# Optimization experiments

Hardware: AMD Instinct MI355X
Metric: run time of the kernel (lower is better)

## Reference

```python
import jax, jax.numpy as jnp
import numpy as np

FEATURE_LIST = [222, 27, 373, 283, 26, 7]
EMB_HID = 6
TN, UN, TF = 2000, 50000, 16


def setup_inputs() -> dict:
    key = jax.random.key(0)
    ks = jax.random.split(key, 4 + len(FEATURE_LIST))
    T_static = jax.random.normal(ks[0], (TN, TF), dtype=jnp.float32)
    # per-column categorical indices, each in-range for its table
    cols = [jax.random.randint(jax.random.fold_in(ks[1], i), (UN,), 0, sz)
            for i, sz in enumerate(FEATURE_LIST)]
    U_static = jnp.stack(cols, axis=1).astype(jnp.int64)  # [UN, 6]
    team_user_matrix = jax.random.randint(ks[2], (TN, UN), 0, 2, dtype=jnp.int32)
    inp = {"T_static": T_static, "U_static": U_static,
           "team_user_matrix": team_user_matrix}
    # embedding tables, xavier_uniform with gain=sqrt(2)
    for i, sz in enumerate(FEATURE_LIST):
        bound = np.sqrt(2.0) * np.sqrt(6.0 / (sz + EMB_HID))
        inp[f"emb{i}"] = jax.random.uniform(ks[3 + i], (sz, EMB_HID),
                                            minval=-bound, maxval=bound,
                                            dtype=jnp.float32)
    return inp


def reference(T_static, U_static, team_user_matrix,
              emb0, emb1, emb2, emb3, emb4, emb5):
    tables = [emb0, emb1, emb2, emb3, emb4, emb5]
    # gather per-feature embeddings and concat -> [UN, 6*emb_hid]
    U_emb = jnp.concatenate(
        [t[U_static[:, i]] for i, t in enumerate(tables)], axis=-1)
    mask = (team_user_matrix == 1).astype(U_emb.dtype)        # [TN, UN]
    counts = jnp.sum(mask, axis=1, keepdims=True)             # [TN, 1]
    # masked mean over each team's users == (mask @ U_emb) / counts
    T_emb = jnp.matmul(mask, U_emb) / counts                  # [TN, 36]
    return jnp.concatenate([T_static, T_emb], axis=-1)        # [TN, TF+36]
```

## Files before the change

kernel.cpp:

```cpp
#include <hip/hip_runtime.h>
#include <hip/hip_bf16.h>

#define TN 2000
#define UN 50000
#define TF 16
#define NCOL 48
#define UNP 50016
#define KSTEPS 1563
#define KCHUNKS 48
#define SPC 33
#define MTILES 125

typedef __attribute__((ext_vector_type(8))) short short8;
typedef __attribute__((ext_vector_type(4))) float f32x4;

__device__ inline unsigned short f2bf(float f) {
    unsigned int x = __float_as_uint(f);
    x += 0x7FFFu + ((x >> 16) & 1u);
    return (unsigned short)(x >> 16);
}

__global__ void build_uembT(const int* __restrict__ U,
                            const float* __restrict__ e0, const float* __restrict__ e1,
                            const float* __restrict__ e2, const float* __restrict__ e3,
                            const float* __restrict__ e4, const float* __restrict__ e5,
                            unsigned short* __restrict__ UT) {
    int u = blockIdx.x * 256 + threadIdx.x;
    if (u >= UNP) return;
    const float* tabs[6] = {e0, e1, e2, e3, e4, e5};
    if (u < UN) {
        #pragma unroll
        for (int f = 0; f < 6; ++f) {
            int idx = U[u * 6 + f];
            #pragma unroll
            for (int h = 0; h < 6; ++h)
                UT[(size_t)(f * 6 + h) * UNP + u] = f2bf(tabs[f][idx * 6 + h]);
        }
        UT[(size_t)36 * UNP + u] = 0x3F80;
    } else {
        #pragma unroll
        for (int c = 0; c < 37; ++c) UT[(size_t)c * UNP + u] = 0;
    }
    #pragma unroll
    for (int c = 37; c < NCOL; ++c) UT[(size_t)c * UNP + u] = 0;
}

__global__ __launch_bounds__(256) void masked_gemm(
        const int* __restrict__ mask, const unsigned short* __restrict__ UT,
        float* __restrict__ accum) {
    int wave = threadIdx.x >> 6;
    int lane = threadIdx.x & 63;
    int mtile = blockIdx.x * 4 + wave;
    if (mtile >= MTILES) return;
    int m0 = mtile * 16;
    int r  = lane & 15;
    int g8 = (lane >> 4) * 8;

    int ks0 = blockIdx.y * SPC;
    int ks1 = ks0 + SPC; if (ks1 > KSTEPS) ks1 = KSTEPS;

    f32x4 acc0 = {0.f, 0.f, 0.f, 0.f};
    f32x4 acc1 = {0.f, 0.f, 0.f, 0.f};
    f32x4 acc2 = {0.f, 0.f, 0.f, 0.f};

    const int* arow = mask + (size_t)(m0 + r) * UN;
    const unsigned short* b0 = UT + (size_t)(r)      * UNP;
    const unsigned short* b1 = UT + (size_t)(r + 16) * UNP;
    const unsigned short* b2 = UT + (size_t)(r + 32) * UNP;

    for (int ks = ks0; ks < ks1; ++ks) {
        int gk = ks * 32 + g8;
        short8 a;
        if (gk < UN) {
            const int4* p = (const int4*)(arow + gk);
            int4 v0 = p[0], v1 = p[1];
            int v[8] = {v0.x, v0.y, v0.z, v0.w, v1.x, v1.y, v1.z, v1.w};
            #pragma unroll
            for (int j = 0; j < 8; ++j) a[j] = (v[j] == 1) ? (short)0x3F80 : (short)0;
        } else {
            #pragma unroll
            for (int j = 0; j < 8; ++j) a[j] = (short)0;
        }
        short8 f0 = *(const short8*)(b0 + gk);
        short8 f1 = *(const short8*)(b1 + gk);
        short8 f2 = *(const short8*)(b2 + gk);
        acc0 = __builtin_amdgcn_mfma_f32_16x16x32_bf16(a, f0, acc0, 0, 0, 0);
        acc1 = __builtin_amdgcn_mfma_f32_16x16x32_bf16(a, f1, acc1, 0, 0, 0);
        acc2 = __builtin_amdgcn_mfma_f32_16x16x32_bf16(a, f2, acc2, 0, 0, 0);
    }

    int row0 = m0 + (lane >> 4) * 4;
    int col  = lane & 15;
    #pragma unroll
    for (int reg = 0; reg < 4; ++reg)
        atomicAdd(&accum[(size_t)(row0 + reg) * NCOL + col], acc0[reg]);
    #pragma unroll
    for (int reg = 0; reg < 4; ++reg)
        atomicAdd(&accum[(size_t)(row0 + reg) * NCOL + col + 16], acc1[reg]);
    if (col < 5) {
        #pragma unroll
        for (int reg = 0; reg < 4; ++reg)
            atomicAdd(&accum[(size_t)(row0 + reg) * NCOL + col + 32], acc2[reg]);
    }
}

__global__ void finalize(const float* __restrict__ T_static,
                         const float* __restrict__ accum,
                         float* __restrict__ out) {
    int t = blockIdx.x;
    int c = threadIdx.x;
    if (c >= TF + 36) return;
    float v;
    if (c < TF) {
        v = T_static[(size_t)t * TF + c];
    } else {
        float cnt = accum[(size_t)t * NCOL + 36];
        v = accum[(size_t)t * NCOL + (c - TF)] / cnt;
    }
    out[(size_t)t * (TF + 36) + c] = v;
}

extern "C" void kernel_launch(void* const* d_in, const int* in_sizes, int n_in,
                              void* d_out, int out_size, void* d_ws, size_t ws_size,
                              hipStream_t stream) {
    const float* T_static = (const float*)d_in[0];
    const int*   U_static = (const int*)d_in[1];
    const int*   mask     = (const int*)d_in[2];
    const float* e0 = (const float*)d_in[3];
    const float* e1 = (const float*)d_in[4];
    const float* e2 = (const float*)d_in[5];
    const float* e3 = (const float*)d_in[6];
    const float* e4 = (const float*)d_in[7];
    const float* e5 = (const float*)d_in[8];
    float* out = (float*)d_out;

    unsigned short* UT = (unsigned short*)d_ws;
    size_t ut_bytes = (size_t)NCOL * UNP * sizeof(unsigned short);
    float* accum = (float*)((char*)d_ws + ut_bytes);

    hipMemsetAsync(accum, 0, (size_t)TN * NCOL * sizeof(float), stream);
    build_uembT<<<dim3((UNP + 255) / 256), dim3(256), 0, stream>>>(
        U_static, e0, e1, e2, e3, e4, e5, UT);
    masked_gemm<<<dim3(32, KCHUNKS), dim3(256), 0, stream>>>(mask, UT, accum);
    finalize<<<dim3(TN), dim3(64), 0, stream>>>(T_static, accum, out);
}
```

Measured before the change: 590.2 us.

## Replace atomics with per-chunk partials, parallelize embedding build, peel tail step

```diff
diff --git a/kernel.cpp b/kernel.cpp
--- a/kernel.cpp
+++ b/kernel.cpp
@@ -7,6 +7,7 @@
 #define NCOL 48
 #define UNP 50016
 #define KSTEPS 1563
+#define KFULL 1562
 #define KCHUNKS 48
 #define SPC 33
 #define MTILES 125
@@ -26,28 +27,37 @@
                             const float* __restrict__ e4, const float* __restrict__ e5,
                             unsigned short* __restrict__ UT) {
     int u = blockIdx.x * 256 + threadIdx.x;
+    int c = blockIdx.y;
     if (u >= UNP) return;
-    const float* tabs[6] = {e0, e1, e2, e3, e4, e5};
+    unsigned short val = 0;
     if (u < UN) {
-        #pragma unroll
-        for (int f = 0; f < 6; ++f) {
+        if (c < 36) {
+            int f = c / 6, h = c - f * 6;
+            const float* t = (f == 0) ? e0 : (f == 1) ? e1 : (f == 2) ? e2
+                           : (f == 3) ? e3 : (f == 4) ? e4 : e5;
             int idx = U[u * 6 + f];
-            #pragma unroll
-            for (int h = 0; h < 6; ++h)
-                UT[(size_t)(f * 6 + h) * UNP + u] = f2bf(tabs[f][idx * 6 + h]);
+            val = f2bf(t[idx * 6 + h]);
+        } else if (c == 36) {
+            val = 0x3F80;
         }
-        UT[(size_t)36 * UNP + u] = 0x3F80;
-    } else {
-        #pragma unroll
-        for (int c = 0; c < 37; ++c) UT[(size_t)c * UNP + u] = 0;
     }
+    UT[(size_t)c * UNP + u] = val;
+}
+
+__device__ inline short8 mask_to_bf16(const int v[8]) {
+    union { short8 s; int i[4]; } a;
     #pragma unroll
-    for (int c = 37; c < NCOL; ++c) UT[(size_t)c * UNP + u] = 0;
+    for (int j = 0; j < 4; ++j) {
+        int lo = (v[2 * j]     == 1) ? 0x3F80     : 0;
+        int hi = (v[2 * j + 1] == 1) ? 0x3F800000 : 0;
+        a.i[j] = lo | hi;
+    }
+    return a.s;
 }
 
 __global__ __launch_bounds__(256) void masked_gemm(
         const int* __restrict__ mask, const unsigned short* __restrict__ UT,
-        float* __restrict__ accum) {
+        float* __restrict__ partial) {
     int wave = threadIdx.x >> 6;
     int lane = threadIdx.x & 63;
     int mtile = blockIdx.x * 4 + wave;
@@ -55,31 +65,43 @@
     int m0 = mtile * 16;
     int r  = lane & 15;
     int g8 = (lane >> 4) * 8;
+    int ky = blockIdx.y;
 
-    int ks0 = blockIdx.y * SPC;
+    int ks0 = ky * SPC;
     int ks1 = ks0 + SPC; if (ks1 > KSTEPS) ks1 = KSTEPS;
+    int ksf = (ks1 < KFULL) ? ks1 : KFULL;
 
     f32x4 acc0 = {0.f, 0.f, 0.f, 0.f};
     f32x4 acc1 = {0.f, 0.f, 0.f, 0.f};
     f32x4 acc2 = {0.f, 0.f, 0.f, 0.f};
 
-    const int* arow = mask + (size_t)(m0 + r) * UN;
-    const unsigned short* b0 = UT + (size_t)(r)      * UNP;
-    const unsigned short* b1 = UT + (size_t)(r + 16) * UNP;
-    const unsigned short* b2 = UT + (size_t)(r + 32) * UNP;
+    const int* arow = mask + (size_t)(m0 + r) * UN + g8;
+    const unsigned short* b0 = UT + (size_t)(r)      * UNP + g8;
+    const unsigned short* b1 = UT + (size_t)(r + 16) * UNP + g8;
+    const unsigned short* b2 = UT + (size_t)(r + 32) * UNP + g8;
 
-    for (int ks = ks0; ks < ks1; ++ks) {
-        int gk = ks * 32 + g8;
-        short8 a;
-        if (gk < UN) {
+    #pragma unroll 3
+    for (int ks = ks0; ks < ksf; ++ks) {
+        int gk = ks * 32;
+        const int4* p = (const int4*)(arow + gk);
+        int4 v0 = p[0], v1 = p[1];
+        int v[8] = {v0.x, v0.y, v0.z, v0.w, v1.x, v1.y, v1.z, v1.w};
+        short8 a  = mask_to_bf16(v);
+        short8 f0 = *(const short8*)(b0 + gk);
+        short8 f1 = *(const short8*)(b1 + gk);
+        short8 f2 = *(const short8*)(b2 + gk);
+        acc0 = __builtin_amdgcn_mfma_f32_16x16x32_bf16(a, f0, acc0, 0, 0, 0);
+        acc1 = __builtin_amdgcn_mfma_f32_16x16x32_bf16(a, f1, acc1, 0, 0, 0);
+        acc2 = __builtin_amdgcn_mfma_f32_16x16x32_bf16(a, f2, acc2, 0, 0, 0);
+    }
+    if (ks1 > KFULL) {
+        int gk = KFULL * 32;
+        short8 a = {0,0,0,0,0,0,0,0};
+        if (g8 < 16) {
             const int4* p = (const int4*)(arow + gk);
             int4 v0 = p[0], v1 = p[1];
             int v[8] = {v0.x, v0.y, v0.z, v0.w, v1.x, v1.y, v1.z, v1.w};
-            #pragma unroll
-            for (int j = 0; j < 8; ++j) a[j] = (v[j] == 1) ? (short)0x3F80 : (short)0;
-        } else {
-            #pragma unroll
-            for (int j = 0; j < 8; ++j) a[j] = (short)0;
+            a = mask_to_bf16(v);
         }
         short8 f0 = *(const short8*)(b0 + gk);
         short8 f1 = *(const short8*)(b1 + gk);
@@ -91,21 +113,18 @@
 
     int row0 = m0 + (lane >> 4) * 4;
     int col  = lane & 15;
+    float* out = partial + ((size_t)ky * TN) * NCOL;
     #pragma unroll
-    for (int reg = 0; reg < 4; ++reg)
-        atomicAdd(&accum[(size_t)(row0 + reg) * NCOL + col], acc0[reg]);
-    #pragma unroll
-    for (int reg = 0; reg < 4; ++reg)
-        atomicAdd(&accum[(size_t)(row0 + reg) * NCOL + col + 16], acc1[reg]);
-    if (col < 5) {
-        #pragma unroll
-        for (int reg = 0; reg < 4; ++reg)
-            atomicAdd(&accum[(size_t)(row0 + reg) * NCOL + col + 32], acc2[reg]);
+    for (int reg = 0; reg < 4; ++reg) {
+        size_t rb = (size_t)(row0 + reg) * NCOL;
+        out[rb + col]      = acc0[reg];
+        out[rb + col + 16] = acc1[reg];
+        out[rb + col + 32] = acc2[reg];
     }
 }
 
 __global__ void finalize(const float* __restrict__ T_static,
-                         const float* __restrict__ accum,
+                         const float* __restrict__ partial,
                          float* __restrict__ out) {
     int t = blockIdx.x;
     int c = threadIdx.x;
@@ -114,8 +133,15 @@
     if (c < TF) {
         v = T_static[(size_t)t * TF + c];
     } else {
-        float cnt = accum[(size_t)t * NCOL + 36];
-        v = accum[(size_t)t * NCOL + (c - TF)] / cnt;
+        int n = c - TF;
+        float s = 0.f, cnt = 0.f;
+        #pragma unroll 4
+        for (int ky = 0; ky < KCHUNKS; ++ky) {
+            const float* row = partial + ((size_t)ky * TN + t) * NCOL;
+            s   += row[n];
+            cnt += row[36];
+        }
+        v = s / cnt;
     }
     out[(size_t)t * (TF + 36) + c] = v;
 }
@@ -136,11 +162,10 @@
 
     unsigned short* UT = (unsigned short*)d_ws;
     size_t ut_bytes = (size_t)NCOL * UNP * sizeof(unsigned short);
-    float* accum = (float*)((char*)d_ws + ut_bytes);
+    float* partial = (float*)((char*)d_ws + ut_bytes);
 
-    hipMemsetAsync(accum, 0, (size_t)TN * NCOL * sizeof(float), stream);
-    build_uembT<<<dim3((UNP + 255) / 256), dim3(256), 0, stream>>>(
+    build_uembT<<<dim3((UNP + 255) / 256, NCOL), dim3(256), 0, stream>>>(
         U_static, e0, e1, e2, e3, e4, e5, UT);
-    masked_gemm<<<dim3(32, KCHUNKS), dim3(256), 0, stream>>>(mask, UT, accum);
-    finalize<<<dim3(TN), dim3(64), 0, stream>>>(T_static, accum, out);
+    masked_gemm<<<dim3(32, KCHUNKS), dim3(256), 0, stream>>>(mask, UT, partial);
+    finalize<<<dim3(TN), dim3(64), 0, stream>>>(T_static, partial, out);
 }
```

Result: no change. 587.5 us (-0.5%).
